# Performance work log

Measured on AMD Instinct MI355X. Metric: run time of the kernel, lower is better.

Reference implementation:

```python
import jax, jax.numpy as jnp
import numpy as np

SCALE = 256.0
QMIN, QMAX = -32768.0, 32767.0
EPS = 1e-5
NUM_HEADS = 16

def fpq(t):
    return jnp.clip(jnp.round(t * SCALE), QMIN, QMAX) / SCALE

def layer_norm(x, g, b):
    mu = jnp.mean(x, axis=-1, keepdims=True)
    var = jnp.mean(jnp.square(x - mu), axis=-1, keepdims=True)
    return (x - mu) * jax.lax.rsqrt(var + EPS) * g + b

def setup_inputs() -> dict:
    key = jax.random.key(0)
    ks = jax.random.split(key, 10)
    B, S, D, H = 8, 1024, 1024, 4096
    s = 1.0 / np.sqrt(D)
    sh = 1.0 / np.sqrt(H)
    return {
        "x": jax.random.normal(ks[0], (B, S, D), jnp.float32),
        "Wqkv": jax.random.uniform(ks[1], (D, 3 * D), jnp.float32, -s, s),
        "bqkv": jax.random.uniform(ks[2], (3 * D,), jnp.float32, -s, s),
        "Wout": jax.random.uniform(ks[3], (D, D), jnp.float32, -s, s),
        "bout": jax.random.uniform(ks[4], (D,), jnp.float32, -s, s),
        "W1": jax.random.uniform(ks[5], (D, H), jnp.float32, -s, s),
        "b1": jax.random.uniform(ks[6], (H,), jnp.float32, -s, s),
        "W2": jax.random.uniform(ks[7], (H, D), jnp.float32, -sh, sh),
        "b2": jax.random.uniform(ks[8], (D,), jnp.float32, -sh, sh),
        "g1": jnp.ones((D,), jnp.float32),
        "beta1": jnp.zeros((D,), jnp.float32),
        "g2": jnp.ones((D,), jnp.float32),
        "beta2": jnp.zeros((D,), jnp.float32),
    }

def reference(x, Wqkv, bqkv, Wout, bout, W1, b1, W2, b2, g1, beta1, g2, beta2):
    B, S, D = x.shape
    Hh = NUM_HEADS
    hd = D // Hh
    # --- attention on norm1(x) ---
    xn = layer_norm(x, g1, beta1)
    qkv = fpq(xn @ Wqkv + bqkv)                       # [B,S,3D]
    q, k, v = jnp.split(qkv, 3, axis=-1)
    q = q.reshape(B, S, Hh, hd).transpose(0, 2, 1, 3)  # [B,H,S,hd]
    k = k.reshape(B, S, Hh, hd).transpose(0, 2, 1, 3)
    v = v.reshape(B, S, Hh, hd).transpose(0, 2, 1, 3)
    scores = jnp.einsum("bhqd,bhkd->bhqk", q, k) / np.sqrt(hd)
    probs = fpq(jax.nn.softmax(scores, axis=-1))
    ctx = jnp.einsum("bhqk,bhkd->bhqd", probs, v)
    ctx = ctx.transpose(0, 2, 1, 3).reshape(B, S, D)
    attn = fpq(ctx @ Wout + bout)
    x = fpq(x + fpq(attn))
    # --- MLP on norm2(x) ---
    xn2 = layer_norm(x, g2, beta2)
    h = jax.nn.relu(fpq(xn2 @ W1 + b1))
    mlp = fpq(h @ W2 + b2)
    x = fpq(x + fpq(mlp))
    return x
```

## Files before the change

### kernel.cpp

```cpp
#include <hip/hip_runtime.h>
#include <hip/hip_fp16.h>
#include <stdint.h>

typedef _Float16 f16;
typedef _Float16 f16x4 __attribute__((ext_vector_type(4)));
typedef _Float16 f16x8 __attribute__((ext_vector_type(8)));
typedef float f32x4 __attribute__((ext_vector_type(4)));

__device__ __forceinline__ float fpq(float t) {
    float r = rintf(t * 256.0f);
    r = fminf(fmaxf(r, -32768.0f), 32767.0f);
    return r * 0.00390625f;
}

__device__ __forceinline__ int swzkey(int r) { return (r & 3) | ((r >> 1) & 4); }

__device__ __forceinline__ void gll16(const f16* g, f16* l) {
    __builtin_amdgcn_global_load_lds(
        (const __attribute__((address_space(1))) uint32_t*)g,
        (__attribute__((address_space(3))) uint32_t*)l, 16, 0, 0);
}

template <int N> __device__ __forceinline__ void waitvm() {
    if constexpr (N == 0)      asm volatile("s_waitcnt vmcnt(0)" ::: "memory");
    else if constexpr (N == 2) asm volatile("s_waitcnt vmcnt(2)" ::: "memory");
    else if constexpr (N == 4) asm volatile("s_waitcnt vmcnt(4)" ::: "memory");
    else if constexpr (N == 6) asm volatile("s_waitcnt vmcnt(6)" ::: "memory");
    else                       asm volatile("s_waitcnt vmcnt(8)" ::: "memory");
}

__global__ __launch_bounds__(256) void ln_kernel(
        const float* __restrict__ x, const float* __restrict__ g,
        const float* __restrict__ b, f16* __restrict__ out) {
    int row = blockIdx.x;
    int t = threadIdx.x;
    const float4* xr = (const float4*)(x + (size_t)row * 1024);
    float4 v = xr[t];
    float s = v.x + v.y + v.z + v.w;
    float s2 = v.x * v.x + v.y * v.y + v.z * v.z + v.w * v.w;
#pragma unroll
    for (int o = 32; o >= 1; o >>= 1) {
        s += __shfl_down(s, o);
        s2 += __shfl_down(s2, o);
    }
    __shared__ float red[8];
    int wid = t >> 6;
    if ((t & 63) == 0) { red[wid] = s; red[4 + wid] = s2; }
    __syncthreads();
    float ts = red[0] + red[1] + red[2] + red[3];
    float ts2 = red[4] + red[5] + red[6] + red[7];
    float mu = ts * (1.0f / 1024.0f);
    float var = ts2 * (1.0f / 1024.0f) - mu * mu;
    float rs = rsqrtf(var + 1e-5f);
    float4 gg = ((const float4*)g)[t];
    float4 bb = ((const float4*)b)[t];
    f16x4 o4;
    o4[0] = (f16)((v.x - mu) * rs * gg.x + bb.x);
    o4[1] = (f16)((v.y - mu) * rs * gg.y + bb.y);
    o4[2] = (f16)((v.z - mu) * rs * gg.z + bb.z);
    o4[3] = (f16)((v.w - mu) * rs * gg.w + bb.w);
    ((f16x4*)out)[(size_t)row * 256 + t] = o4;
}

__global__ __launch_bounds__(256) void transpose_kernel(
        const float* __restrict__ W, f16* __restrict__ WT, int K, int N) {
    __shared__ float tile[32][33];
    int n0 = blockIdx.x * 32, k0 = blockIdx.y * 32;
    int tx = threadIdx.x & 31, ty = threadIdx.x >> 5;
#pragma unroll
    for (int i = 0; i < 32; i += 8)
        tile[ty + i][tx] = W[(size_t)(k0 + ty + i) * N + n0 + tx];
    __syncthreads();
#pragma unroll
    for (int i = 0; i < 32; i += 8)
        WT[(size_t)(n0 + ty + i) * K + k0 + tx] = (f16)tile[tx][ty + i];
}

template <int EPI, int BN>
__global__ __launch_bounds__(512, 2) void gemm8_kernel(
        const f16* __restrict__ A, const f16* __restrict__ BT,
        int N, int K, int GM, int GN,
        const float* __restrict__ bias, const float* __restrict__ resid,
        void* __restrict__ out0, f16* __restrict__ outk, f16* __restrict__ outv) {
    constexpr int WN = (BN == 256) ? 4 : 2;
    constexpr int MF = (BN == 256) ? 8 : 4;
    constexpr int GB = BN / 64;
    constexpr int ABUF = 256 * 64;
    constexpr int BBUF = BN * 64;
    constexpr int BUFSZ = ABUF + BBUF;
    __shared__ f16 lds[2 * BUFSZ];

    int nwg = GM * GN;
    int orig = blockIdx.x;
    int wg = (orig & 7) * (nwg >> 3) + (orig >> 3);
    int bn = wg % GN, bm = wg / GN;
    int m0 = bm * 256, n0 = bn * BN;
    int tid = threadIdx.x;
    int lane = tid & 63;
    int lr = lane & 15, lg = lane >> 4;
    int wv = tid >> 6;
    int wm = wv / WN, wn = wv % WN;

    size_t srcA[4]; int dstA[4];
#pragma unroll
    for (int j = 0; j < 4; ++j) {
        int row = j * 64 + (tid >> 3);
        int slot = (tid & 7) ^ (row & 7);
        srcA[j] = (size_t)(m0 + row) * K + slot * 8;
        dstA[j] = j * 4096 + tid * 8;
    }
    size_t srcB[GB]; int dstB[GB];
#pragma unroll
    for (int j = 0; j < GB; ++j) {
        int row = j * 64 + (tid >> 3);
        int slot = (tid & 7) ^ (row & 7);
        srcB[j] = (size_t)(n0 + row) * K + slot * 8;
        dstB[j] = j * 4096 + tid * 8;
    }

    int offA[2][MF], offB[4][2];
#pragma unroll
    for (int i = 0; i < MF; ++i) {
        int row = wm * (MF * 16) + i * 16 + lr;
#pragma unroll
        for (int kk = 0; kk < 2; ++kk)
            offA[kk][i] = row * 64 + (((kk * 4 + lg) ^ (row & 7)) * 8);
    }
#pragma unroll
    for (int j = 0; j < 4; ++j) {
        int n = wn * 64 + j * 16 + lr;
#pragma unroll
        for (int kk = 0; kk < 2; ++kk)
            offB[j][kk] = ABUF + n * 64 + (((kk * 4 + lg) ^ (n & 7)) * 8);
    }

    f32x4 acc[MF][4] = {};
    int NT = K >> 6;

#pragma unroll
    for (int j = 0; j < 4; ++j) gll16(A + srcA[j], lds + dstA[j]);
#pragma unroll
    for (int j = 0; j < GB; ++j) gll16(BT + srcB[j], lds + ABUF + dstB[j]);
#pragma unroll
    for (int j = 0; j < 4; ++j) gll16(A + srcA[j] + 64, lds + BUFSZ + dstA[j]);
#pragma unroll
    for (int j = 0; j < GB; ++j) gll16(BT + srcB[j] + 64, lds + BUFSZ + ABUF + dstB[j]);
    if constexpr (BN == 256) { waitvm<8>(); } else { waitvm<6>(); }
    __builtin_amdgcn_s_barrier();
    __builtin_amdgcn_sched_barrier(0);

    for (int t = 0; t < NT; ++t) {
        int cur = t & 1;
        f16* Ab = lds + cur * BUFSZ;
        f16x8 a0[MF], a1[MF], b00, b01, b10, b11;
#pragma unroll
        for (int i = 0; i < MF; ++i) a0[i] = *(const f16x8*)&Ab[offA[0][i]];
        b00 = *(const f16x8*)&Ab[offB[0][0]];
        b01 = *(const f16x8*)&Ab[offB[1][0]];
#pragma unroll
        for (int i = 0; i < MF; ++i) a1[i] = *(const f16x8*)&Ab[offA[1][i]];
        b10 = *(const f16x8*)&Ab[offB[0][1]];
        b11 = *(const f16x8*)&Ab[offB[1][1]];
        __builtin_amdgcn_s_setprio(1);
#pragma unroll
        for (int i = 0; i < MF; ++i) {
            acc[i][0] = __builtin_amdgcn_mfma_f32_16x16x32_f16(a0[i], b00, acc[i][0], 0, 0, 0);
            acc[i][1] = __builtin_amdgcn_mfma_f32_16x16x32_f16(a0[i], b01, acc[i][1], 0, 0, 0);
        }
#pragma unroll
        for (int i = 0; i < MF; ++i) {
            acc[i][0] = __builtin_amdgcn_mfma_f32_16x16x32_f16(a1[i], b10, acc[i][0], 0, 0, 0);
            acc[i][1] = __builtin_amdgcn_mfma_f32_16x16x32_f16(a1[i], b11, acc[i][1], 0, 0, 0);
        }
        __builtin_amdgcn_s_setprio(0);
        f16x8 b20 = *(const f16x8*)&Ab[offB[2][0]];
        f16x8 b30 = *(const f16x8*)&Ab[offB[3][0]];
        f16x8 b21 = *(const f16x8*)&Ab[offB[2][1]];
        f16x8 b31 = *(const f16x8*)&Ab[offB[3][1]];
        asm volatile("s_waitcnt lgkmcnt(0)" ::: "memory");
        __builtin_amdgcn_sched_barrier(0);
        __builtin_amdgcn_s_barrier();
        if (t + 2 < NT) {
            size_t kof = (size_t)(t + 2) << 6;
            f16* Bd = Ab + ABUF;
#pragma unroll
            for (int j = 0; j < 4; ++j) gll16(A + srcA[j] + kof, Ab + dstA[j]);
#pragma unroll
            for (int j = 0; j < GB; ++j) gll16(BT + srcB[j] + kof, Bd + dstB[j]);
        }
        __builtin_amdgcn_s_setprio(1);
#pragma unroll
        for (int i = 0; i < MF; ++i) {
            acc[i][2] = __builtin_amdgcn_mfma_f32_16x16x32_f16(a0[i], b20, acc[i][2], 0, 0, 0);
            acc[i][3] = __builtin_amdgcn_mfma_f32_16x16x32_f16(a0[i], b30, acc[i][3], 0, 0, 0);
        }
#pragma unroll
        for (int i = 0; i < MF; ++i) {
            acc[i][2] = __builtin_amdgcn_mfma_f32_16x16x32_f16(a1[i], b21, acc[i][2], 0, 0, 0);
            acc[i][3] = __builtin_amdgcn_mfma_f32_16x16x32_f16(a1[i], b31, acc[i][3], 0, 0, 0);
        }
        __builtin_amdgcn_s_setprio(0);
        if (t + 2 < NT) {
            if constexpr (BN == 256) { waitvm<8>(); } else { waitvm<6>(); }
        } else if (t + 1 < NT) {
            waitvm<0>();
        }
        __builtin_amdgcn_sched_barrier(0);
        __builtin_amdgcn_s_barrier();
    }

#pragma unroll
    for (int i = 0; i < MF; ++i) {
#pragma unroll
        for (int j = 0; j < 4; ++j) {
            int col = n0 + wn * 64 + j * 16 + lr;
            float bv = bias[col];
#pragma unroll
            for (int r = 0; r < 4; ++r) {
                int row = m0 + wm * (MF * 16) + i * 16 + lg * 4 + r;
                float val = acc[i][j][r] + bv;
                if (EPI == 0) {
                    float qv = fpq(val);
                    int part = col >> 10, wi = col & 1023;
                    int hd = wi >> 6, d = wi & 63;
                    int bb = row >> 10, ss = row & 1023;
                    size_t bh = (size_t)(bb * 16 + hd);
                    if (part == 0) {
                        ((f16*)out0)[(bh * 1024 + ss) * 64 + d] = (f16)qv;
                    } else if (part == 1) {
                        outk[bh * 65536 + (ss >> 6) * 4096 + (ss & 63) * 64 + (d ^ (swzkey(ss) << 3))] = (f16)qv;
                    } else {
                        outv[bh * 65536 + (ss >> 6) * 4096 + d * 64 + ((ss & 63) ^ (swzkey(d) << 3))] = (f16)qv;
                    }
                } else if (EPI == 2) {
                    float hv = fmaxf(fpq(val), 0.0f);
                    ((f16*)out0)[(size_t)row * N + col] = (f16)hv;
                } else {
                    float o = fpq(resid[(size_t)row * 1024 + col] + fpq(val));
                    ((float*)out0)[(size_t)row * 1024 + col] = o;
                }
            }
        }
    }
}

__global__ __launch_bounds__(256) void attn_kernel(
        const f16* __restrict__ Q, const f16* __restrict__ Kg,
        const f16* __restrict__ Vt, f16* __restrict__ ctx) {
    int id = blockIdx.x;
    int qt = (id >> 3) & 15;
    int bh = (id >> 7) * 8 + (id & 7);
    int b = bh >> 4, h = bh & 15;
    const f16* Qp = Q + ((size_t)bh * 1024 + (size_t)qt * 64) * 64;
    const f16* Kp = Kg + (size_t)bh * 65536;
    const f16* Vp = Vt + (size_t)bh * 65536;
    int t = threadIdx.x, lane = t & 63, w = t >> 6;
    int lr = lane & 15, lg = lane >> 4;
    __shared__ f16 Ks[2][4096];
    __shared__ f16 Vs[2][4096];
    int so = t * 8;

    const float L2E = 1.4426950408889634f;
    const float C0 = -24.0f * 1.4426950408889634f;

    f16x8 qf[2];
#pragma unroll
    for (int kk = 0; kk < 2; ++kk) {
        qf[kk] = *(const f16x8*)(Qp + (w * 16 + lr) * 64 + kk * 32 + lg * 8);
#pragma unroll
        for (int j = 0; j < 8; ++j) qf[kk][j] = qf[kk][j] * (f16)0.125f;
    }
    int koff[4][2], voff[4][2];
#pragma unroll
    for (int nf = 0; nf < 4; ++nf) {
        int rowv = 32 * (nf >> 1) + 8 * ((lr >> 2) ^ (2 * (nf & 1))) + 4 * (nf & 1) + (lr & 3);
#pragma unroll
        for (int kk = 0; kk < 2; ++kk)
            koff[nf][kk] = rowv * 64 + (((kk * 4 + lg) ^ swzkey(rowv)) * 8);
    }
#pragma unroll
    for (int db = 0; db < 4; ++db) {
        int d = db * 16 + lr;
#pragma unroll
        for (int kk = 0; kk < 2; ++kk)
            voff[db][kk] = d * 64 + (((kk * 4 + lg) ^ swzkey(d)) * 8);
    }

    gll16(Kp + so, Ks[0] + so);
    gll16(Kp + 2048 + so, Ks[0] + 2048 + so);
    float lsum = 0.0f;
    for (int kt = 0; kt < 16; ++kt) {
        int cur = kt & 1;
        if (kt < 15) {
            const f16* src = Kp + (kt + 1) * 4096;
            gll16(src + so, Ks[cur ^ 1] + so);
            gll16(src + 2048 + so, Ks[cur ^ 1] + 2048 + so);
            waitvm<2>();
        } else {
            waitvm<0>();
        }
        __builtin_amdgcn_sched_barrier(0);
        __builtin_amdgcn_s_barrier();
        f32x4 sc[4] = {};
#pragma unroll
        for (int kk = 0; kk < 2; ++kk)
#pragma unroll
            for (int nf = 0; nf < 4; ++nf) {
                f16x8 kf = *(const f16x8*)&Ks[cur][koff[nf][kk]];
                sc[nf] = __builtin_amdgcn_mfma_f32_16x16x32_f16(kf, qf[kk], sc[nf], 0, 0, 0);
            }
        float part = 0.0f;
#pragma unroll
        for (int nf = 0; nf < 4; ++nf)
#pragma unroll
            for (int r = 0; r < 4; ++r)
                part += __builtin_amdgcn_exp2f(fmaf(sc[nf][r], L2E, C0));
        lsum += part;
        __builtin_amdgcn_s_barrier();
    }
    lsum += __shfl_xor(lsum, 16);
    lsum += __shfl_xor(lsum, 32);
    float rl256 = 256.0f * __builtin_amdgcn_rcpf(lsum);

    f32x4 co[4] = {};
    const float inv256 = 0.00390625f;
    gll16(Kp + so, Ks[0] + so);
    gll16(Kp + 2048 + so, Ks[0] + 2048 + so);
    gll16(Vp + so, Vs[0] + so);
    gll16(Vp + 2048 + so, Vs[0] + 2048 + so);
    for (int kt = 0; kt < 16; ++kt) {
        int cur = kt & 1;
        if (kt < 15) {
            const f16* srck = Kp + (kt + 1) * 4096;
            const f16* srcv = Vp + (kt + 1) * 4096;
            gll16(srck + so, Ks[cur ^ 1] + so);
            gll16(srck + 2048 + so, Ks[cur ^ 1] + 2048 + so);
            gll16(srcv + so, Vs[cur ^ 1] + so);
            gll16(srcv + 2048 + so, Vs[cur ^ 1] + 2048 + so);
            waitvm<4>();
        } else {
            waitvm<0>();
        }
        __builtin_amdgcn_sched_barrier(0);
        __builtin_amdgcn_s_barrier();
        f32x4 sc[4] = {};
#pragma unroll
        for (int kk = 0; kk < 2; ++kk)
#pragma unroll
            for (int nf = 0; nf < 4; ++nf) {
                f16x8 kf = *(const f16x8*)&Ks[cur][koff[nf][kk]];
                sc[nf] = __builtin_amdgcn_mfma_f32_16x16x32_f16(kf, qf[kk], sc[nf], 0, 0, 0);
            }
        uint32_t pk0[4], pk1[4];
#pragma unroll
        for (int nf = 0; nf < 4; ++nf) {
            float e0 = __builtin_amdgcn_exp2f(fmaf(sc[nf][0], L2E, C0));
            float e1 = __builtin_amdgcn_exp2f(fmaf(sc[nf][1], L2E, C0));
            float e2 = __builtin_amdgcn_exp2f(fmaf(sc[nf][2], L2E, C0));
            float e3 = __builtin_amdgcn_exp2f(fmaf(sc[nf][3], L2E, C0));
            float r0 = rintf(e0 * rl256);
            float r1 = rintf(e1 * rl256);
            float r2 = rintf(e2 * rl256);
            float r3 = rintf(e3 * rl256);
            pk0[nf] = __builtin_bit_cast(uint32_t,
                        __builtin_amdgcn_cvt_pkrtz(r0 * inv256, r1 * inv256));
            pk1[nf] = __builtin_bit_cast(uint32_t,
                        __builtin_amdgcn_cvt_pkrtz(r2 * inv256, r3 * inv256));
        }
#pragma unroll
        for (int kk = 0; kk < 2; ++kk) {
            uint4 fw;
            fw.x = pk0[2 * kk];
            fw.y = pk1[2 * kk];
            fw.z = __shfl_xor(pk0[2 * kk + 1], 32);
            fw.w = __shfl_xor(pk1[2 * kk + 1], 32);
            f16x8 pa = __builtin_bit_cast(f16x8, fw);
#pragma unroll
            for (int db = 0; db < 4; ++db) {
                f16x8 vb = *(const f16x8*)&Vs[cur][voff[db][kk]];
                co[db] = __builtin_amdgcn_mfma_f32_16x16x32_f16(pa, vb, co[db], 0, 0, 0);
            }
        }
        __builtin_amdgcn_s_barrier();
    }
#pragma unroll
    for (int db = 0; db < 4; ++db)
#pragma unroll
        for (int r = 0; r < 4; ++r) {
            int ss = qt * 64 + w * 16 + lg * 4 + r;
            ctx[((size_t)b * 1024 + ss) * 1024 + h * 64 + db * 16 + lr] = (f16)co[db][r];
        }
}

extern "C" void kernel_launch(void* const* d_in, const int* in_sizes, int n_in,
                              void* d_out, int out_size, void* d_ws, size_t ws_size,
                              hipStream_t stream) {
    const float* x     = (const float*)d_in[0];
    const float* Wqkv  = (const float*)d_in[1];
    const float* bqkv  = (const float*)d_in[2];
    const float* Wout  = (const float*)d_in[3];
    const float* bout  = (const float*)d_in[4];
    const float* W1    = (const float*)d_in[5];
    const float* b1    = (const float*)d_in[6];
    const float* W2    = (const float*)d_in[7];
    const float* b2    = (const float*)d_in[8];
    const float* g1    = (const float*)d_in[9];
    const float* beta1 = (const float*)d_in[10];
    const float* g2    = (const float*)d_in[11];
    const float* beta2 = (const float*)d_in[12];

    char* ws = (char*)d_ws;
    const size_t MB = 1ull << 20;
    f16*  q_h   = (f16*)(ws);
    f16*  k_h   = (f16*)(ws + 16 * MB);
    f16*  vt_h  = (f16*)(ws + 32 * MB);
    f16*  ctx_h = (f16*)(ws + 48 * MB);
    f16*  h_h   = (f16*)(ws);
    f16*  xn_h  = (f16*)(ws + 64 * MB);
    float* x1   = (float*)(ws + 80 * MB);
    f16*  wT    = (f16*)(ws + 112 * MB);

    ln_kernel<<<8192, 256, 0, stream>>>(x, g1, beta1, xn_h);
    transpose_kernel<<<dim3(96, 32), 256, 0, stream>>>(Wqkv, wT, 1024, 3072);
    gemm8_kernel<0, 256><<<384, 512, 0, stream>>>(xn_h, wT, 3072, 1024, 32, 12, bqkv, nullptr, q_h, k_h, vt_h);
    attn_kernel<<<2048, 256, 0, stream>>>(q_h, k_h, vt_h, ctx_h);
    transpose_kernel<<<dim3(32, 32), 256, 0, stream>>>(Wout, wT, 1024, 1024);
    gemm8_kernel<1, 128><<<256, 512, 0, stream>>>(ctx_h, wT, 1024, 1024, 32, 8, bout, x, x1, nullptr, nullptr);
    ln_kernel<<<8192, 256, 0, stream>>>(x1, g2, beta2, xn_h);
    transpose_kernel<<<dim3(128, 32), 256, 0, stream>>>(W1, wT, 1024, 4096);
    gemm8_kernel<2, 256><<<512, 512, 0, stream>>>(xn_h, wT, 4096, 1024, 32, 16, b1, nullptr, h_h, nullptr, nullptr);
    transpose_kernel<<<dim3(32, 128), 256, 0, stream>>>(W2, wT, 4096, 1024);
    gemm8_kernel<3, 128><<<256, 512, 0, stream>>>(h_h, wT, 1024, 4096, 32, 8, b2, x1, d_out, nullptr, nullptr);
}
```

Before: 386.5 us.

## Restructure BN=256 GEMM main loop into four-phase quadrant schedule with split prefetch

For the BN=256 GEMM variant, each K-step is split into four MFMA quadrants (A rows 0-3 and 4-7 crossed with B columns 0-1 and 2-3). LDS fragment loads are interleaved between the quadrants, and the next-tile B and A global-to-LDS prefetches are issued at separate points. The goal is to overlap LDS reads and global loads with MFMA work and to reduce register pressure, since only half of the A fragments are live at a time. It adds several more workgroup barriers per iteration, which could cost more in synchronisation than the overlap recovers. The BN=128 path is unchanged.

```diff
diff --git a/kernel.cpp b/kernel.cpp
--- a/kernel.cpp
+++ b/kernel.cpp
@@ -137,76 +137,176 @@
     f32x4 acc[MF][4] = {};
     int NT = K >> 6;
 
-#pragma unroll
-    for (int j = 0; j < 4; ++j) gll16(A + srcA[j], lds + dstA[j]);
-#pragma unroll
-    for (int j = 0; j < GB; ++j) gll16(BT + srcB[j], lds + ABUF + dstB[j]);
-#pragma unroll
-    for (int j = 0; j < 4; ++j) gll16(A + srcA[j] + 64, lds + BUFSZ + dstA[j]);
-#pragma unroll
-    for (int j = 0; j < GB; ++j) gll16(BT + srcB[j] + 64, lds + BUFSZ + ABUF + dstB[j]);
-    if constexpr (BN == 256) { waitvm<8>(); } else { waitvm<6>(); }
-    __builtin_amdgcn_s_barrier();
-    __builtin_amdgcn_sched_barrier(0);
-
-    for (int t = 0; t < NT; ++t) {
-        int cur = t & 1;
-        f16* Ab = lds + cur * BUFSZ;
-        f16x8 a0[MF], a1[MF], b00, b01, b10, b11;
-#pragma unroll
-        for (int i = 0; i < MF; ++i) a0[i] = *(const f16x8*)&Ab[offA[0][i]];
-        b00 = *(const f16x8*)&Ab[offB[0][0]];
-        b01 = *(const f16x8*)&Ab[offB[1][0]];
-#pragma unroll
-        for (int i = 0; i < MF; ++i) a1[i] = *(const f16x8*)&Ab[offA[1][i]];
-        b10 = *(const f16x8*)&Ab[offB[0][1]];
-        b11 = *(const f16x8*)&Ab[offB[1][1]];
-        __builtin_amdgcn_s_setprio(1);
-#pragma unroll
-        for (int i = 0; i < MF; ++i) {
-            acc[i][0] = __builtin_amdgcn_mfma_f32_16x16x32_f16(a0[i], b00, acc[i][0], 0, 0, 0);
-            acc[i][1] = __builtin_amdgcn_mfma_f32_16x16x32_f16(a0[i], b01, acc[i][1], 0, 0, 0);
-        }
-#pragma unroll
-        for (int i = 0; i < MF; ++i) {
-            acc[i][0] = __builtin_amdgcn_mfma_f32_16x16x32_f16(a1[i], b10, acc[i][0], 0, 0, 0);
-            acc[i][1] = __builtin_amdgcn_mfma_f32_16x16x32_f16(a1[i], b11, acc[i][1], 0, 0, 0);
-        }
-        __builtin_amdgcn_s_setprio(0);
-        f16x8 b20 = *(const f16x8*)&Ab[offB[2][0]];
-        f16x8 b30 = *(const f16x8*)&Ab[offB[3][0]];
-        f16x8 b21 = *(const f16x8*)&Ab[offB[2][1]];
-        f16x8 b31 = *(const f16x8*)&Ab[offB[3][1]];
-        asm volatile("s_waitcnt lgkmcnt(0)" ::: "memory");
+    if constexpr (BN == 256) {
+#pragma unroll
+        for (int j = 0; j < 4; ++j) gll16(A + srcA[j], lds + dstA[j]);
+#pragma unroll
+        for (int j = 0; j < 4; ++j) gll16(BT + srcB[j], lds + ABUF + dstB[j]);
+#pragma unroll
+        for (int j = 0; j < 4; ++j) gll16(A + srcA[j] + 64, lds + BUFSZ + dstA[j]);
+#pragma unroll
+        for (int j = 0; j < 4; ++j) gll16(BT + srcB[j] + 64, lds + BUFSZ + ABUF + dstB[j]);
+        waitvm<8>();
+        __builtin_amdgcn_s_barrier();
         __builtin_amdgcn_sched_barrier(0);
+
+        for (int t = 0; t < NT; ++t) {
+            f16* C = lds + (t & 1) * BUFSZ;
+            bool s2 = (t + 2 < NT);
+            size_t k2 = (size_t)(t + 2) << 6;
+            f16x8 a0[4][2], a1[4][2], bq0[2][2], bq1[2][2];
+#pragma unroll
+            for (int i = 0; i < 4; ++i) {
+                a0[i][0] = *(const f16x8*)&C[offA[0][i]];
+                a0[i][1] = *(const f16x8*)&C[offA[1][i]];
+            }
+#pragma unroll
+            for (int j = 0; j < 2; ++j) {
+                bq0[j][0] = *(const f16x8*)&C[offB[j][0]];
+                bq0[j][1] = *(const f16x8*)&C[offB[j][1]];
+            }
+            __builtin_amdgcn_s_barrier();
+            asm volatile("s_waitcnt lgkmcnt(0)" ::: "memory");
+            __builtin_amdgcn_sched_barrier(0);
+            __builtin_amdgcn_s_setprio(1);
+#pragma unroll
+            for (int i = 0; i < 4; ++i)
+#pragma unroll
+                for (int j = 0; j < 2; ++j) {
+                    acc[i][j] = __builtin_amdgcn_mfma_f32_16x16x32_f16(a0[i][0], bq0[j][0], acc[i][j], 0, 0, 0);
+                    acc[i][j] = __builtin_amdgcn_mfma_f32_16x16x32_f16(a0[i][1], bq0[j][1], acc[i][j], 0, 0, 0);
+                }
+            __builtin_amdgcn_s_setprio(0);
+            __builtin_amdgcn_s_barrier();
+#pragma unroll
+            for (int j = 0; j < 2; ++j) {
+                bq1[j][0] = *(const f16x8*)&C[offB[2 + j][0]];
+                bq1[j][1] = *(const f16x8*)&C[offB[2 + j][1]];
+            }
+            __builtin_amdgcn_s_barrier();
+            asm volatile("s_waitcnt lgkmcnt(0)" ::: "memory");
+            __builtin_amdgcn_sched_barrier(0);
+            __builtin_amdgcn_s_setprio(1);
+#pragma unroll
+            for (int i = 0; i < 4; ++i)
+#pragma unroll
+                for (int j = 0; j < 2; ++j) {
+                    acc[i][2 + j] = __builtin_amdgcn_mfma_f32_16x16x32_f16(a0[i][0], bq1[j][0], acc[i][2 + j], 0, 0, 0);
+                    acc[i][2 + j] = __builtin_amdgcn_mfma_f32_16x16x32_f16(a0[i][1], bq1[j][1], acc[i][2 + j], 0, 0, 0);
+                }
+            __builtin_amdgcn_s_setprio(0);
+            __builtin_amdgcn_s_barrier();
+#pragma unroll
+            for (int i = 0; i < 4; ++i) {
+                a1[i][0] = *(const f16x8*)&C[offA[0][4 + i]];
+                a1[i][1] = *(const f16x8*)&C[offA[1][4 + i]];
+            }
+            if (s2) {
+#pragma unroll
+                for (int j = 0; j < 4; ++j)
+                    gll16(BT + srcB[j] + k2, C + ABUF + dstB[j]);
+            }
+            __builtin_amdgcn_s_barrier();
+            asm volatile("s_waitcnt lgkmcnt(0)" ::: "memory");
+            __builtin_amdgcn_sched_barrier(0);
+            __builtin_amdgcn_s_setprio(1);
+#pragma unroll
+            for (int i = 0; i < 4; ++i)
+#pragma unroll
+                for (int j = 0; j < 2; ++j) {
+                    acc[4 + i][j] = __builtin_amdgcn_mfma_f32_16x16x32_f16(a1[i][0], bq0[j][0], acc[4 + i][j], 0, 0, 0);
+                    acc[4 + i][j] = __builtin_amdgcn_mfma_f32_16x16x32_f16(a1[i][1], bq0[j][1], acc[4 + i][j], 0, 0, 0);
+                }
+            __builtin_amdgcn_s_setprio(0);
+            __builtin_amdgcn_s_barrier();
+            if (s2) {
+#pragma unroll
+                for (int j = 0; j < 4; ++j)
+                    gll16(A + srcA[j] + k2, C + dstA[j]);
+            }
+            __builtin_amdgcn_s_setprio(1);
+#pragma unroll
+            for (int i = 0; i < 4; ++i)
+#pragma unroll
+                for (int j = 0; j < 2; ++j) {
+                    acc[4 + i][2 + j] = __builtin_amdgcn_mfma_f32_16x16x32_f16(a1[i][0], bq1[j][0], acc[4 + i][2 + j], 0, 0, 0);
+                    acc[4 + i][2 + j] = __builtin_amdgcn_mfma_f32_16x16x32_f16(a1[i][1], bq1[j][1], acc[4 + i][2 + j], 0, 0, 0);
+                }
+            __builtin_amdgcn_s_setprio(0);
+            if (s2) { waitvm<8>(); }
+            else if (t + 1 < NT) { waitvm<0>(); }
+            __builtin_amdgcn_sched_barrier(0);
+            __builtin_amdgcn_s_barrier();
+        }
+    } else {
+#pragma unroll
+        for (int j = 0; j < 4; ++j) gll16(A + srcA[j], lds + dstA[j]);
+#pragma unroll
+        for (int j = 0; j < GB; ++j) gll16(BT + srcB[j], lds + ABUF + dstB[j]);
+#pragma unroll
+        for (int j = 0; j < 4; ++j) gll16(A + srcA[j] + 64, lds + BUFSZ + dstA[j]);
+#pragma unroll
+        for (int j = 0; j < GB; ++j) gll16(BT + srcB[j] + 64, lds + BUFSZ + ABUF + dstB[j]);
+        waitvm<6>();
         __builtin_amdgcn_s_barrier();
-        if (t + 2 < NT) {
-            size_t kof = (size_t)(t + 2) << 6;
-            f16* Bd = Ab + ABUF;
-#pragma unroll
-            for (int j = 0; j < 4; ++j) gll16(A + srcA[j] + kof, Ab + dstA[j]);
-#pragma unroll
-            for (int j = 0; j < GB; ++j) gll16(BT + srcB[j] + kof, Bd + dstB[j]);
-        }
-        __builtin_amdgcn_s_setprio(1);
-#pragma unroll
-        for (int i = 0; i < MF; ++i) {
-            acc[i][2] = __builtin_amdgcn_mfma_f32_16x16x32_f16(a0[i], b20, acc[i][2], 0, 0, 0);
-            acc[i][3] = __builtin_amdgcn_mfma_f32_16x16x32_f16(a0[i], b30, acc[i][3], 0, 0, 0);
-        }
-#pragma unroll
-        for (int i = 0; i < MF; ++i) {
-            acc[i][2] = __builtin_amdgcn_mfma_f32_16x16x32_f16(a1[i], b21, acc[i][2], 0, 0, 0);
-            acc[i][3] = __builtin_amdgcn_mfma_f32_16x16x32_f16(a1[i], b31, acc[i][3], 0, 0, 0);
-        }
-        __builtin_amdgcn_s_setprio(0);
-        if (t + 2 < NT) {
-            if constexpr (BN == 256) { waitvm<8>(); } else { waitvm<6>(); }
-        } else if (t + 1 < NT) {
-            waitvm<0>();
-        }
         __builtin_amdgcn_sched_barrier(0);
-        __builtin_amdgcn_s_barrier();
+
+        for (int t = 0; t < NT; ++t) {
+            int cur = t & 1;
+            f16* Ab = lds + cur * BUFSZ;
+            f16x8 a0[MF], a1[MF], b00, b01, b10, b11;
+#pragma unroll
+            for (int i = 0; i < MF; ++i) a0[i] = *(const f16x8*)&Ab[offA[0][i]];
+            b00 = *(const f16x8*)&Ab[offB[0][0]];
+            b01 = *(const f16x8*)&Ab[offB[1][0]];
+#pragma unroll
+            for (int i = 0; i < MF; ++i) a1[i] = *(const f16x8*)&Ab[offA[1][i]];
+            b10 = *(const f16x8*)&Ab[offB[0][1]];
+            b11 = *(const f16x8*)&Ab[offB[1][1]];
+            __builtin_amdgcn_s_setprio(1);
+#pragma unroll
+            for (int i = 0; i < MF; ++i) {
+                acc[i][0] = __builtin_amdgcn_mfma_f32_16x16x32_f16(a0[i], b00, acc[i][0], 0, 0, 0);
+                acc[i][1] = __builtin_amdgcn_mfma_f32_16x16x32_f16(a0[i], b01, acc[i][1], 0, 0, 0);
+            }
+#pragma unroll
+            for (int i = 0; i < MF; ++i) {
+                acc[i][0] = __builtin_amdgcn_mfma_f32_16x16x32_f16(a1[i], b10, acc[i][0], 0, 0, 0);
+                acc[i][1] = __builtin_amdgcn_mfma_f32_16x16x32_f16(a1[i], b11, acc[i][1], 0, 0, 0);
+            }
+            __builtin_amdgcn_s_setprio(0);
+            f16x8 b20 = *(const f16x8*)&Ab[offB[2][0]];
+            f16x8 b30 = *(const f16x8*)&Ab[offB[3][0]];
+            f16x8 b21 = *(const f16x8*)&Ab[offB[2][1]];
+            f16x8 b31 = *(const f16x8*)&Ab[offB[3][1]];
+            asm volatile("s_waitcnt lgkmcnt(0)" ::: "memory");
+            __builtin_amdgcn_sched_barrier(0);
+            __builtin_amdgcn_s_barrier();
+            if (t + 2 < NT) {
+                size_t kof = (size_t)(t + 2) << 6;
+                f16* Bd = Ab + ABUF;
+#pragma unroll
+                for (int j = 0; j < 4; ++j) gll16(A + srcA[j] + kof, Ab + dstA[j]);
+#pragma unroll
+                for (int j = 0; j < GB; ++j) gll16(BT + srcB[j] + kof, Bd + dstB[j]);
+            }
+            __builtin_amdgcn_s_setprio(1);
+#pragma unroll
+            for (int i = 0; i < MF; ++i) {
+                acc[i][2] = __builtin_amdgcn_mfma_f32_16x16x32_f16(a0[i], b20, acc[i][2], 0, 0, 0);
+                acc[i][3] = __builtin_amdgcn_mfma_f32_16x16x32_f16(a0[i], b30, acc[i][3], 0, 0, 0);
+            }
+#pragma unroll
+            for (int i = 0; i < MF; ++i) {
+                acc[i][2] = __builtin_amdgcn_mfma_f32_16x16x32_f16(a1[i], b21, acc[i][2], 0, 0, 0);
+                acc[i][3] = __builtin_amdgcn_mfma_f32_16x16x32_f16(a1[i], b31, acc[i][3], 0, 0, 0);
+            }
+            __builtin_amdgcn_s_setprio(0);
+            if (t + 2 < NT) { waitvm<6>(); }
+            else if (t + 1 < NT) { waitvm<0>(); }
+            __builtin_amdgcn_sched_barrier(0);
+            __builtin_amdgcn_s_barrier();
+        }
     }
 
 #pragma unroll
```

Measured after the change: 388.6 us. No clear change (+0.5%).

## Replace double-buffered 256-row GEMM with simple 128x128 single-buffer GEMM

Applied to the files above, without the earlier changes.

Replaces the tuned double-buffered 256xBN GEMM (512 threads, BK=64, async LDS prefetch two steps ahead, setprio interleaving) with a plain 128x128 tile kernel. The new kernel uses 256 threads, BK=32 and a single LDS buffer with two syncthreads per k-step, and requests 3 blocks per CU. The goal is more workgroups and higher occupancy. In exchange it gives up the overlap of loads with MFMA and per-tile data reuse, so it risks exposing load latency and adding barrier stalls.

```diff
diff --git a/kernel.cpp b/kernel.cpp
--- a/kernel.cpp
+++ b/kernel.cpp
@@ -14,6 +14,7 @@
 }
 
 __device__ __forceinline__ int swzkey(int r) { return (r & 3) | ((r >> 1) & 4); }
+__device__ __forceinline__ int kk2(int r) { return (r >> 1) & 3; }
 
 __device__ __forceinline__ void gll16(const f16* g, f16* l) {
     __builtin_amdgcn_global_load_lds(
@@ -76,148 +77,77 @@
         WT[(size_t)(n0 + ty + i) * K + k0 + tx] = (f16)tile[tx][ty + i];
 }
 
-template <int EPI, int BN>
-__global__ __launch_bounds__(512, 2) void gemm8_kernel(
+template <int EPI>
+__global__ __launch_bounds__(256, 3) void gemm97_kernel(
         const f16* __restrict__ A, const f16* __restrict__ BT,
         int N, int K, int GM, int GN,
         const float* __restrict__ bias, const float* __restrict__ resid,
         void* __restrict__ out0, f16* __restrict__ outk, f16* __restrict__ outv) {
-    constexpr int WN = (BN == 256) ? 4 : 2;
-    constexpr int MF = (BN == 256) ? 8 : 4;
-    constexpr int GB = BN / 64;
-    constexpr int ABUF = 256 * 64;
-    constexpr int BBUF = BN * 64;
-    constexpr int BUFSZ = ABUF + BBUF;
-    __shared__ f16 lds[2 * BUFSZ];
+    constexpr int ABUF = 128 * 32;
+    __shared__ f16 lds[2 * ABUF];
 
     int nwg = GM * GN;
     int orig = blockIdx.x;
     int wg = (orig & 7) * (nwg >> 3) + (orig >> 3);
     int bn = wg % GN, bm = wg / GN;
-    int m0 = bm * 256, n0 = bn * BN;
+    int m0 = bm * 128, n0 = bn * 128;
     int tid = threadIdx.x;
     int lane = tid & 63;
     int lr = lane & 15, lg = lane >> 4;
     int wv = tid >> 6;
-    int wm = wv / WN, wn = wv % WN;
-
-    size_t srcA[4]; int dstA[4];
-#pragma unroll
-    for (int j = 0; j < 4; ++j) {
-        int row = j * 64 + (tid >> 3);
-        int slot = (tid & 7) ^ (row & 7);
+    int wm = wv >> 1, wn = wv & 1;
+
+    size_t srcA[2], srcB[2];
+#pragma unroll
+    for (int j = 0; j < 2; ++j) {
+        int row = j * 64 + (tid >> 2);
+        int slot = (tid & 3) ^ kk2(row);
         srcA[j] = (size_t)(m0 + row) * K + slot * 8;
-        dstA[j] = j * 4096 + tid * 8;
-    }
-    size_t srcB[GB]; int dstB[GB];
-#pragma unroll
-    for (int j = 0; j < GB; ++j) {
-        int row = j * 64 + (tid >> 3);
-        int slot = (tid & 7) ^ (row & 7);
         srcB[j] = (size_t)(n0 + row) * K + slot * 8;
-        dstB[j] = j * 4096 + tid * 8;
-    }
-
-    int offA[2][MF], offB[4][2];
-#pragma unroll
-    for (int i = 0; i < MF; ++i) {
-        int row = wm * (MF * 16) + i * 16 + lr;
-#pragma unroll
-        for (int kk = 0; kk < 2; ++kk)
-            offA[kk][i] = row * 64 + (((kk * 4 + lg) ^ (row & 7)) * 8);
-    }
-#pragma unroll
-    for (int j = 0; j < 4; ++j) {
-        int n = wn * 64 + j * 16 + lr;
-#pragma unroll
-        for (int kk = 0; kk < 2; ++kk)
-            offB[j][kk] = ABUF + n * 64 + (((kk * 4 + lg) ^ (n & 7)) * 8);
-    }
-
-    f32x4 acc[MF][4] = {};
-    int NT = K >> 6;
-
-#pragma unroll
-    for (int j = 0; j < 4; ++j) gll16(A + srcA[j], lds + dstA[j]);
-#pragma unroll
-    for (int j = 0; j < GB; ++j) gll16(BT + srcB[j], lds + ABUF + dstB[j]);
-#pragma unroll
-    for (int j = 0; j < 4; ++j) gll16(A + srcA[j] + 64, lds + BUFSZ + dstA[j]);
-#pragma unroll
-    for (int j = 0; j < GB; ++j) gll16(BT + srcB[j] + 64, lds + BUFSZ + ABUF + dstB[j]);
-    if constexpr (BN == 256) { waitvm<8>(); } else { waitvm<6>(); }
-    __builtin_amdgcn_s_barrier();
-    __builtin_amdgcn_sched_barrier(0);
+    }
+    int dst0 = tid * 8, dst1 = 2048 + tid * 8;
+
+    int offA[4], offB[4];
+#pragma unroll
+    for (int i = 0; i < 4; ++i) {
+        int row = wm * 64 + i * 16 + lr;
+        offA[i] = row * 32 + ((lg ^ kk2(row)) * 8);
+        int n = wn * 64 + i * 16 + lr;
+        offB[i] = ABUF + n * 32 + ((lg ^ kk2(n)) * 8);
+    }
+
+    f32x4 acc[4][4] = {};
+    int NT = K >> 5;
 
     for (int t = 0; t < NT; ++t) {
-        int cur = t & 1;
-        f16* Ab = lds + cur * BUFSZ;
-        f16x8 a0[MF], a1[MF], b00, b01, b10, b11;
-#pragma unroll
-        for (int i = 0; i < MF; ++i) a0[i] = *(const f16x8*)&Ab[offA[0][i]];
-        b00 = *(const f16x8*)&Ab[offB[0][0]];
-        b01 = *(const f16x8*)&Ab[offB[1][0]];
-#pragma unroll
-        for (int i = 0; i < MF; ++i) a1[i] = *(const f16x8*)&Ab[offA[1][i]];
-        b10 = *(const f16x8*)&Ab[offB[0][1]];
-        b11 = *(const f16x8*)&Ab[offB[1][1]];
-        __builtin_amdgcn_s_setprio(1);
-#pragma unroll
-        for (int i = 0; i < MF; ++i) {
-            acc[i][0] = __builtin_amdgcn_mfma_f32_16x16x32_f16(a0[i], b00, acc[i][0], 0, 0, 0);
-            acc[i][1] = __builtin_amdgcn_mfma_f32_16x16x32_f16(a0[i], b01, acc[i][1], 0, 0, 0);
-        }
-#pragma unroll
-        for (int i = 0; i < MF; ++i) {
-            acc[i][0] = __builtin_amdgcn_mfma_f32_16x16x32_f16(a1[i], b10, acc[i][0], 0, 0, 0);
-            acc[i][1] = __builtin_amdgcn_mfma_f32_16x16x32_f16(a1[i], b11, acc[i][1], 0, 0, 0);
-        }
-        __builtin_amdgcn_s_setprio(0);
-        f16x8 b20 = *(const f16x8*)&Ab[offB[2][0]];
-        f16x8 b30 = *(const f16x8*)&Ab[offB[3][0]];
-        f16x8 b21 = *(const f16x8*)&Ab[offB[2][1]];
-        f16x8 b31 = *(const f16x8*)&Ab[offB[3][1]];
-        asm volatile("s_waitcnt lgkmcnt(0)" ::: "memory");
-        __builtin_amdgcn_sched_barrier(0);
-        __builtin_amdgcn_s_barrier();
-        if (t + 2 < NT) {
-            size_t kof = (size_t)(t + 2) << 6;
-            f16* Bd = Ab + ABUF;
-#pragma unroll
-            for (int j = 0; j < 4; ++j) gll16(A + srcA[j] + kof, Ab + dstA[j]);
-#pragma unroll
-            for (int j = 0; j < GB; ++j) gll16(BT + srcB[j] + kof, Bd + dstB[j]);
-        }
-        __builtin_amdgcn_s_setprio(1);
-#pragma unroll
-        for (int i = 0; i < MF; ++i) {
-            acc[i][2] = __builtin_amdgcn_mfma_f32_16x16x32_f16(a0[i], b20, acc[i][2], 0, 0, 0);
-            acc[i][3] = __builtin_amdgcn_mfma_f32_16x16x32_f16(a0[i], b30, acc[i][3], 0, 0, 0);
-        }
-#pragma unroll
-        for (int i = 0; i < MF; ++i) {
-            acc[i][2] = __builtin_amdgcn_mfma_f32_16x16x32_f16(a1[i], b21, acc[i][2], 0, 0, 0);
-            acc[i][3] = __builtin_amdgcn_mfma_f32_16x16x32_f16(a1[i], b31, acc[i][3], 0, 0, 0);
-        }
-        __builtin_amdgcn_s_setprio(0);
-        if (t + 2 < NT) {
-            if constexpr (BN == 256) { waitvm<8>(); } else { waitvm<6>(); }
-        } else if (t + 1 < NT) {
-            waitvm<0>();
-        }
-        __builtin_amdgcn_sched_barrier(0);
-        __builtin_amdgcn_s_barrier();
-    }
-
-#pragma unroll
-    for (int i = 0; i < MF; ++i) {
+        size_t kof = (size_t)t << 5;
+        __syncthreads();
+        gll16(A + srcA[0] + kof, lds + dst0);
+        gll16(A + srcA[1] + kof, lds + dst1);
+        gll16(BT + srcB[0] + kof, lds + ABUF + dst0);
+        gll16(BT + srcB[1] + kof, lds + ABUF + dst1);
+        __syncthreads();
+        f16x8 af[4], bf[4];
+#pragma unroll
+        for (int i = 0; i < 4; ++i) af[i] = *(const f16x8*)&lds[offA[i]];
+#pragma unroll
+        for (int j = 0; j < 4; ++j) bf[j] = *(const f16x8*)&lds[offB[j]];
+#pragma unroll
+        for (int i = 0; i < 4; ++i)
+#pragma unroll
+            for (int j = 0; j < 4; ++j)
+                acc[i][j] = __builtin_amdgcn_mfma_f32_16x16x32_f16(af[i], bf[j], acc[i][j], 0, 0, 0);
+    }
+
+#pragma unroll
+    for (int i = 0; i < 4; ++i) {
 #pragma unroll
         for (int j = 0; j < 4; ++j) {
             int col = n0 + wn * 64 + j * 16 + lr;
             float bv = bias[col];
 #pragma unroll
             for (int r = 0; r < 4; ++r) {
-                int row = m0 + wm * (MF * 16) + i * 16 + lg * 4 + r;
+                int row = m0 + wm * 64 + i * 16 + lg * 4 + r;
                 float val = acc[i][j][r] + bv;
                 if (EPI == 0) {
                     float qv = fpq(val);
@@ -422,13 +352,13 @@
 
     ln_kernel<<<8192, 256, 0, stream>>>(x, g1, beta1, xn_h);
     transpose_kernel<<<dim3(96, 32), 256, 0, stream>>>(Wqkv, wT, 1024, 3072);
-    gemm8_kernel<0, 256><<<384, 512, 0, stream>>>(xn_h, wT, 3072, 1024, 32, 12, bqkv, nullptr, q_h, k_h, vt_h);
+    gemm97_kernel<0><<<1536, 256, 0, stream>>>(xn_h, wT, 3072, 1024, 64, 24, bqkv, nullptr, q_h, k_h, vt_h);
     attn_kernel<<<2048, 256, 0, stream>>>(q_h, k_h, vt_h, ctx_h);
     transpose_kernel<<<dim3(32, 32), 256, 0, stream>>>(Wout, wT, 1024, 1024);
-    gemm8_kernel<1, 128><<<256, 512, 0, stream>>>(ctx_h, wT, 1024, 1024, 32, 8, bout, x, x1, nullptr, nullptr);
+    gemm97_kernel<1><<<512, 256, 0, stream>>>(ctx_h, wT, 1024, 1024, 64, 8, bout, x, x1, nullptr, nullptr);
     ln_kernel<<<8192, 256, 0, stream>>>(x1, g2, beta2, xn_h);
     transpose_kernel<<<dim3(128, 32), 256, 0, stream>>>(W1, wT, 1024, 4096);
-    gemm8_kernel<2, 256><<<512, 512, 0, stream>>>(xn_h, wT, 4096, 1024, 32, 16, b1, nullptr, h_h, nullptr, nullptr);
+    gemm97_kernel<2><<<2048, 256, 0, stream>>>(xn_h, wT, 4096, 1024, 64, 32, b1, nullptr, h_h, nullptr, nullptr);
     transpose_kernel<<<dim3(32, 128), 256, 0, stream>>>(W2, wT, 4096, 1024);
-    gemm8_kernel<3, 128><<<256, 512, 0, stream>>>(h_h, wT, 1024, 4096, 32, 8, b2, x1, d_out, nullptr, nullptr);
-}
+    gemm97_kernel<3><<<512, 256, 0, stream>>>(h_h, wT, 1024, 4096, 64, 8, b2, x1, d_out, nullptr, nullptr);
+}
```

Measured after the change: 401.7 us. 1.04x slower.
